# Optimization experiments

Measured on AMD Instinct MI355X. Metric: run time of the kernel, lower is better.

## Reference

```python
import jax, jax.numpy as jnp
import numpy as np

N_NODES = 50000
N_EDGES = 800000
NFEAT, NHID, NCLASS = 512, 128, 64


def setup_inputs() -> dict:
    key = jax.random.key(0)
    ks = jax.random.split(key, 8)
    x = jax.random.normal(ks[0], (N_NODES, NFEAT), dtype=jnp.float32)
    # GraphConvolution params (uniform-ish init like reset_parameters, stdv = 1/sqrt(fan_out))
    W1 = jax.random.normal(ks[1], (NFEAT, NHID), dtype=jnp.float32) * (1.0 / np.sqrt(NHID))
    b1 = jnp.zeros((NHID,), dtype=jnp.float32)
    W2 = jax.random.normal(ks[2], (NHID, NCLASS), dtype=jnp.float32) * (1.0 / np.sqrt(NCLASS))
    b2 = jnp.zeros((NCLASS,), dtype=jnp.float32)
    # sparse normalized adjacency in COO form
    edge_row = jax.random.randint(ks[3], (N_EDGES,), 0, N_NODES, dtype=jnp.int32)
    edge_col = jax.random.randint(ks[4], (N_EDGES,), 0, N_NODES, dtype=jnp.int32)
    edge_val = jax.random.uniform(ks[5], (N_EDGES,), dtype=jnp.float32) * 0.1
    return {"x": x, "W1": W1, "b1": b1, "W2": W2, "b2": b2,
            "edge_val": edge_val, "edge_row": edge_row, "edge_col": edge_col}


def _spmm(feat, edge_row, edge_col, edge_val, n_nodes):
    # (adj @ feat) with adj given as COO: out[r] = sum_e val[e] * feat[c[e]]
    msg = feat[edge_col] * edge_val[:, None]          # [E, d]
    return jax.ops.segment_sum(msg, edge_row, num_segments=n_nodes)


def reference(x, W1, b1, W2, b2, edge_val, edge_row, edge_col):
    # eval mode: dropout = identity, use_bn = False
    n = x.shape[0]
    h = jax.nn.relu(_spmm(x @ W1, edge_row, edge_col, edge_val, n) + b1)  # gc1 + relu
    out = _spmm(h @ W2, edge_row, edge_col, edge_val, n) + b2             # gc2
    return out
```

## Files before the change

### kernel.cpp

```cpp
#include <hip/hip_runtime.h>

#define N_NODES 50000
#define N_EDGES 800000
#define NFEAT 512
#define NHID 128
#define NCLASS 64

#define SCAN_BLOCKS 49
#define ZERO_BLOCKS 49

using bf16x8 = __attribute__((ext_vector_type(8))) __bf16;
using f32x4  = __attribute__((ext_vector_type(4))) float;
using u16x8  = __attribute__((ext_vector_type(8))) unsigned short;
using u16x4  = __attribute__((ext_vector_type(4))) unsigned short;
typedef unsigned long long u64;

__device__ __forceinline__ unsigned short f2bf(float f)
{
    unsigned u = __builtin_bit_cast(unsigned, f);
    unsigned r = (u + 0x7FFFu + ((u >> 16) & 1u)) >> 16;
    return (unsigned short)r;
}
__device__ __forceinline__ float bf2f(unsigned short b)
{
    return __builtin_bit_cast(float, (unsigned)b << 16);
}
__device__ __forceinline__ u16x4 cvt4(float4 f)
{
    u16x4 h;
    h[0] = __builtin_bit_cast(unsigned short, (__bf16)f.x);
    h[1] = __builtin_bit_cast(unsigned short, (__bf16)f.y);
    h[2] = __builtin_bit_cast(unsigned short, (__bf16)f.z);
    h[3] = __builtin_bit_cast(unsigned short, (__bf16)f.w);
    return h;
}

__global__ void prep_kernel(int4* __restrict__ zp, int n4,
                            const float* __restrict__ W1, const float* __restrict__ W2,
                            unsigned short* __restrict__ W1t, unsigned short* __restrict__ W2t)
{
    const int b = blockIdx.x;
    if (b < ZERO_BLOCKS) {
        const int i = b * 256 + threadIdx.x;
        if (i < n4) zp[i] = make_int4(0, 0, 0, 0);
    } else {
        const int idx = (b - ZERO_BLOCKS) * 256 + threadIdx.x;
        if (idx < NFEAT * NHID) {
            const int n = idx / NFEAT, k = idx % NFEAT;
            W1t[idx] = f2bf(W1[k * NHID + n]);
        } else {
            const int j = idx - NFEAT * NHID;
            if (j < NHID * NCLASS) {
                const int n = j / NHID, k = j % NHID;
                W2t[j] = f2bf(W2[k * NCLASS + n]);
            }
        }
    }
}

__global__ __launch_bounds__(512) void gemm1_pipe(const float* __restrict__ A,
                                                  const unsigned short* __restrict__ Bt,
                                                  unsigned short* __restrict__ C, int M)
{
    constexpr int K = NFEAT, N = NHID, BM = 128, BK = 32, NSTEP = K / BK;
    constexpr int LDW = BK + 8;
    __shared__ unsigned short As[2][BM][LDW];
    __shared__ unsigned short Bs[2][N][LDW];

    const int tid  = threadIdx.x;
    const int wid  = tid >> 6;
    const int lane = tid & 63;
    const int lm   = lane & 15;
    const int lk   = (lane >> 4) * 8;
    const int m0   = blockIdx.x * BM;

    const int ar0 = tid >> 3;
    const int ac0 = (tid & 7) * 4;
    const int ga0 = (m0 + ar0      < M) ? (m0 + ar0)      : (M - 1);
    const int ga1 = (m0 + ar0 + 64 < M) ? (m0 + ar0 + 64) : (M - 1);
    const float* Arow0 = &A[(size_t)ga0 * K];
    const float* Arow1 = &A[(size_t)ga1 * K];
    const int bn = tid >> 2;
    const int bk = (tid & 3) * 8;
    const unsigned short* Brow = &Bt[(size_t)bn * K];

    f32x4 acc[8] = {};

    {
        float4 fa0 = *(const float4*)&Arow0[ac0];
        float4 fa1 = *(const float4*)&Arow1[ac0];
        u16x8  bv  = *(const u16x8*)&Brow[bk];
        *(u16x4*)&As[0][ar0][ac0]      = cvt4(fa0);
        *(u16x4*)&As[0][ar0 + 64][ac0] = cvt4(fa1);
        *(u16x8*)&Bs[0][bn][bk]        = bv;
    }
    __syncthreads();

    #pragma unroll
    for (int t = 0; t < NSTEP; ++t) {
        const int cur = t & 1;
        float4 na0, na1; u16x8 nb;
        if (t + 1 < NSTEP) {
            na0 = *(const float4*)&Arow0[(t + 1) * BK + ac0];
            na1 = *(const float4*)&Arow1[(t + 1) * BK + ac0];
            nb  = *(const u16x8*)&Brow[(t + 1) * BK + bk];
        }
        bf16x8 a = __builtin_bit_cast(bf16x8, *(const u16x8*)&As[cur][wid * 16 + lm][lk]);
        #pragma unroll
        for (int nf = 0; nf < 8; ++nf) {
            bf16x8 b = __builtin_bit_cast(bf16x8, *(const u16x8*)&Bs[cur][nf * 16 + lm][lk]);
            acc[nf] = __builtin_amdgcn_mfma_f32_16x16x32_bf16(a, b, acc[nf], 0, 0, 0);
        }
        if (t + 1 < NSTEP) {
            *(u16x4*)&As[cur ^ 1][ar0][ac0]      = cvt4(na0);
            *(u16x4*)&As[cur ^ 1][ar0 + 64][ac0] = cvt4(na1);
            *(u16x8*)&Bs[cur ^ 1][bn][bk]        = nb;
            __syncthreads();
        }
    }

    #pragma unroll
    for (int nf = 0; nf < 8; ++nf)
        #pragma unroll
        for (int r = 0; r < 4; ++r) {
            const int m = m0 + wid * 16 + (lane >> 4) * 4 + r;
            if (m < M) C[(size_t)m * N + nf * 16 + lm] =
                __builtin_bit_cast(unsigned short, (__bf16)acc[nf][r]);
        }
}

template<int K, int N>
__global__ __launch_bounds__(256) void gemm_mfma_bf16a(const unsigned short* __restrict__ A,
                                                       const unsigned short* __restrict__ Bt,
                                                       unsigned short* __restrict__ C, int M)
{
    constexpr int BM = 128, BK = 32, NF = N / 16;
    constexpr int LDW = BK + 8;
    __shared__ unsigned short As[BM][LDW];
    __shared__ unsigned short Bs[N][LDW];

    const int tid  = threadIdx.x;
    const int wid  = tid >> 6;
    const int lane = tid & 63;
    const int lm   = lane & 15;
    const int lk   = (lane >> 4) * 8;
    const int m0   = blockIdx.x * BM;

    f32x4 acc[2][NF] = {};

    for (int k0 = 0; k0 < K; k0 += BK) {
        if (k0) __syncthreads();
        {
            #pragma unroll
            for (int c = 0; c < 2; ++c) {
                const int chunk = tid * 2 + c;
                const int r  = chunk >> 2;
                const int kc = (chunk & 3) * 8;
                const int m  = m0 + r;
                u16x8 v = {};
                if (m < M) v = *(const u16x8*)&A[(size_t)m * K + k0 + kc];
                *(u16x8*)&As[r][kc] = v;
            }
        }
        {
            constexpr int CH  = (N * BK / 8) / 256;
            constexpr int CPR = BK / 8;
            #pragma unroll
            for (int c = 0; c < CH; ++c) {
                const int chunk = tid * CH + c;
                const int n  = chunk / CPR;
                const int kc = (chunk % CPR) * 8;
                *(u16x8*)&Bs[n][kc] = *(const u16x8*)&Bt[(size_t)n * K + k0 + kc];
            }
        }
        __syncthreads();

        bf16x8 a[2];
        #pragma unroll
        for (int mf = 0; mf < 2; ++mf)
            a[mf] = __builtin_bit_cast(bf16x8, *(const u16x8*)&As[wid * 32 + mf * 16 + lm][lk]);
        #pragma unroll
        for (int nf = 0; nf < NF; ++nf) {
            bf16x8 b = __builtin_bit_cast(bf16x8, *(const u16x8*)&Bs[nf * 16 + lm][lk]);
            #pragma unroll
            for (int mf = 0; mf < 2; ++mf)
                acc[mf][nf] = __builtin_amdgcn_mfma_f32_16x16x32_bf16(a[mf], b, acc[mf][nf], 0, 0, 0);
        }
    }

    #pragma unroll
    for (int mf = 0; mf < 2; ++mf)
        #pragma unroll
        for (int nf = 0; nf < NF; ++nf)
            #pragma unroll
            for (int r = 0; r < 4; ++r) {
                const int m = m0 + wid * 32 + mf * 16 + (lane >> 4) * 4 + r;
                if (m < M) C[(size_t)m * N + nf * 16 + lm] =
                    __builtin_bit_cast(unsigned short, (__bf16)acc[mf][nf][r]);
            }
}

__global__ void hist_rank_kernel(const int* __restrict__ er, int* __restrict__ counts,
                                 unsigned char* __restrict__ rank)
{
    int e = blockIdx.x * blockDim.x + threadIdx.x;
    if (e < N_EDGES) rank[e] = (unsigned char)atomicAdd(&counts[er[e]], 1);
}

__global__ __launch_bounds__(1024) void scan_blocks(const int* __restrict__ counts,
                                                    int* __restrict__ row_ptr,
                                                    int* __restrict__ bsums)
{
    __shared__ int tmp[1024];
    const int tid = threadIdx.x;
    const int gid = blockIdx.x * 1024 + tid;
    const int v = (gid < N_NODES) ? counts[gid] : 0;
    tmp[tid] = v;
    __syncthreads();
    #pragma unroll
    for (int off = 1; off < 1024; off <<= 1) {
        int t = (tid >= off) ? tmp[tid - off] : 0;
        __syncthreads();
        tmp[tid] += t;
        __syncthreads();
    }
    if (gid < N_NODES) row_ptr[gid] = tmp[tid] - v;
    if (tid == 1023) bsums[blockIdx.x] = tmp[1023];
}

__global__ void scan_bsums(int* __restrict__ bsums)
{
    const int lane = threadIdx.x;
    const int orig = (lane < SCAN_BLOCKS) ? bsums[lane] : 0;
    int v = orig;
    #pragma unroll
    for (int off = 1; off < 64; off <<= 1) {
        int t = __shfl_up(v, off, 64);
        if (lane >= off) v += t;
    }
    if (lane < SCAN_BLOCKS) bsums[lane] = v - orig;
}

__global__ __launch_bounds__(1024) void add_offsets(int* __restrict__ row_ptr,
                                                    const int* __restrict__ bsums)
{
    const int gid = blockIdx.x * 1024 + threadIdx.x;
    if (gid < N_NODES) row_ptr[gid] += bsums[blockIdx.x];
    if (gid == 0) row_ptr[N_NODES] = N_EDGES;
}

__global__ void scatter_cv(const int* __restrict__ er, const int* __restrict__ ec,
                           const float* __restrict__ ev, const unsigned char* __restrict__ rank,
                           const int* __restrict__ row_ptr, unsigned* __restrict__ cv)
{
    int e = blockIdx.x * blockDim.x + threadIdx.x;
    if (e >= N_EDGES) return;
    const int r = er[e];
    const int pos = row_ptr[r] + (int)rank[e];
    cv[pos] = ((unsigned)f2bf(ev[e]) << 16) | (unsigned)ec[e];
}

__global__ __launch_bounds__(256) void spmm_bf16_h(const unsigned short* __restrict__ feat,
                                                   const int* __restrict__ row_ptr,
                                                   const unsigned* __restrict__ cv,
                                                   const float* __restrict__ bias,
                                                   unsigned short* __restrict__ out)
{
    const int wave = blockIdx.x * (blockDim.x >> 6) + (threadIdx.x >> 6);
    const int lane = threadIdx.x & 63;
    if (wave >= N_NODES) return;
    const int beg = row_ptr[wave];
    const int end = row_ptr[wave + 1];
    const int deg = end - beg;
    const int n1 = deg < 64 ? deg : 64;

    float ax[8] = {}, ay[8] = {};
    unsigned pcv = 0;
    if (lane < n1) pcv = cv[beg + lane];

    int u = 0;
    for (; u + 7 < n1; u += 8) {
        unsigned pp[8], ww[8];
        #pragma unroll
        for (int j = 0; j < 8; ++j) pp[j] = __shfl(pcv, u + j, 64);
        #pragma unroll
        for (int j = 0; j < 8; ++j)
            ww[j] = *(const unsigned*)&feat[(size_t)(pp[j] & 0xFFFFu) * NHID + lane * 2];
        #pragma unroll
        for (int j = 0; j < 8; ++j) {
            const float v = bf2f((unsigned short)(pp[j] >> 16));
            ax[j] += v * bf2f((unsigned short)(ww[j] & 0xFFFF));
            ay[j] += v * bf2f((unsigned short)(ww[j] >> 16));
        }
    }
    for (; u < n1; ++u) {
        const unsigned p = __shfl(pcv, u, 64);
        const float v = bf2f((unsigned short)(p >> 16));
        const unsigned w = *(const unsigned*)&feat[(size_t)(p & 0xFFFFu) * NHID + lane * 2];
        ax[u & 7] += v * bf2f((unsigned short)(w & 0xFFFF));
        ay[u & 7] += v * bf2f((unsigned short)(w >> 16));
    }
    for (int i = beg + 64; i < end; ++i) {
        const unsigned p = cv[i];
        const float v = bf2f((unsigned short)(p >> 16));
        const unsigned w = *(const unsigned*)&feat[(size_t)(p & 0xFFFFu) * NHID + lane * 2];
        ax[i & 7] += v * bf2f((unsigned short)(w & 0xFFFF));
        ay[i & 7] += v * bf2f((unsigned short)(w >> 16));
    }
    const float sx = ((ax[0] + ax[1]) + (ax[2] + ax[3])) + ((ax[4] + ax[5]) + (ax[6] + ax[7]));
    const float sy = ((ay[0] + ay[1]) + (ay[2] + ay[3])) + ((ay[4] + ay[5]) + (ay[6] + ay[7]));
    const float2 bb = *(const float2*)&bias[lane * 2];
    const float rx = fmaxf(sx + bb.x, 0.f);
    const float ry = fmaxf(sy + bb.y, 0.f);
    const unsigned pack = (unsigned)f2bf(rx) | ((unsigned)f2bf(ry) << 16);
    *(unsigned*)&out[(size_t)wave * NHID + lane * 2] = pack;
}

__global__ __launch_bounds__(256) void spmm_bf16_o(const unsigned short* __restrict__ feat,
                                                   const int* __restrict__ row_ptr,
                                                   const unsigned* __restrict__ cv,
                                                   const float* __restrict__ bias,
                                                   float* __restrict__ out)
{
    const int wave = blockIdx.x * (blockDim.x >> 6) + (threadIdx.x >> 6);
    const int lane = threadIdx.x & 63;
    if (wave >= N_NODES) return;
    const int beg = row_ptr[wave];
    const int end = row_ptr[wave + 1];
    const int deg = end - beg;
    const int n1 = deg < 64 ? deg : 64;

    float a[8] = {};
    unsigned pcv = 0;
    if (lane < n1) pcv = cv[beg + lane];

    int u = 0;
    for (; u + 7 < n1; u += 8) {
        unsigned pp[8]; unsigned short ww[8];
        #pragma unroll
        for (int j = 0; j < 8; ++j) pp[j] = __shfl(pcv, u + j, 64);
        #pragma unroll
        for (int j = 0; j < 8; ++j)
            ww[j] = feat[(size_t)(pp[j] & 0xFFFFu) * NCLASS + lane];
        #pragma unroll
        for (int j = 0; j < 8; ++j)
            a[j] += bf2f((unsigned short)(pp[j] >> 16)) * bf2f(ww[j]);
    }
    for (; u < n1; ++u) {
        const unsigned p = __shfl(pcv, u, 64);
        a[u & 7] += bf2f((unsigned short)(p >> 16)) * bf2f(feat[(size_t)(p & 0xFFFFu) * NCLASS + lane]);
    }
    for (int i = beg + 64; i < end; ++i) {
        const unsigned p = cv[i];
        a[i & 7] += bf2f((unsigned short)(p >> 16)) * bf2f(feat[(size_t)(p & 0xFFFFu) * NCLASS + lane]);
    }
    const float s = ((a[0] + a[1]) + (a[2] + a[3])) + ((a[4] + a[5]) + (a[6] + a[7]));
    out[(size_t)wave * NCLASS + lane] = s + bias[lane];
}

extern "C" void kernel_launch(void* const* d_in, const int* in_sizes, int n_in,
                              void* d_out, int out_size, void* d_ws, size_t ws_size,
                              hipStream_t stream)
{
    const float* x  = (const float*)d_in[0];
    const float* W1 = (const float*)d_in[1];
    const float* b1 = (const float*)d_in[2];
    const float* W2 = (const float*)d_in[3];
    const float* b2 = (const float*)d_in[4];
    const float* ev = (const float*)d_in[5];
    const int*   er = (const int*)d_in[6];
    const int*   ec = (const int*)d_in[7];
    float* out = (float*)d_out;

    unsigned* cv = (unsigned*)d_ws;
    unsigned char* rank = (unsigned char*)(cv + N_EDGES);
    unsigned short* XW1  = (unsigned short*)(rank + N_EDGES);
    unsigned short* Hpre = XW1 + (size_t)N_NODES * NHID;
    int* row_ptr = (int*)(Hpre + (size_t)N_NODES * NHID);
    int* counts  = row_ptr + 50016;
    int* bsums   = counts + 50016;
    unsigned short* W1t = (unsigned short*)(bsums + 64);
    unsigned short* W2t = W1t + NFEAT * NHID;

    unsigned short* HW2 = XW1;

    {
        const int n4 = (50016 + 64) / 4;
        const int conv_blocks = (NFEAT * NHID + NHID * NCLASS + 255) / 256;
        prep_kernel<<<ZERO_BLOCKS + conv_blocks, 256, 0, stream>>>(
            (int4*)counts, n4, W1, W2, W1t, W2t);
    }
    hist_rank_kernel<<<(N_EDGES + 255) / 256, 256, 0, stream>>>(er, counts, rank);
    scan_blocks<<<SCAN_BLOCKS, 1024, 0, stream>>>(counts, row_ptr, bsums);
    scan_bsums<<<1, 64, 0, stream>>>(bsums);
    add_offsets<<<SCAN_BLOCKS, 1024, 0, stream>>>(row_ptr, bsums);
    scatter_cv<<<(N_EDGES + 255) / 256, 256, 0, stream>>>(er, ec, ev, rank, row_ptr, cv);

    gemm1_pipe<<<(N_NODES + 127) / 128, 512, 0, stream>>>(x, W1t, XW1, N_NODES);
    spmm_bf16_h<<<(N_NODES + 3) / 4, 256, 0, stream>>>(XW1, row_ptr, cv, b1, Hpre);
    gemm_mfma_bf16a<NHID, NCLASS><<<(N_NODES + 127) / 128, 256, 0, stream>>>(Hpre, W2t, HW2, N_NODES);
    spmm_bf16_o<<<(N_NODES + 3) / 4, 256, 0, stream>>>(HW2, row_ptr, cv, b2, out);
}
```

Measured before the change: 164.2 us.

## Split SpMM lanes across edges with vectorized gathers; fuse block-sum scan into offset add

Both SpMM kernels now give each lane a 4-element (8-byte) slice of a feature row, so several edges are gathered per wave instruction (2 edges per wave for the hidden layer, 4 for the output layer). Partial sums are then combined with cross-lane shuffles. This cuts the number of gather instructions and shuffle broadcasts per edge and widens each memory access. The single-block bsums scan is folded into each add_offsets block, which drops one kernel launch at the cost of redundant per-block scans. The trade-off is extra reduction shuffles, masked lanes when degree is not a multiple of the group width, and half of the lanes sitting idle during the store.

```diff
diff --git a/kernel.cpp b/kernel.cpp
--- a/kernel.cpp
+++ b/kernel.cpp
@@ -228,24 +228,24 @@
     if (tid == 1023) bsums[blockIdx.x] = tmp[1023];
 }
 
-__global__ void scan_bsums(int* __restrict__ bsums)
-{
-    const int lane = threadIdx.x;
-    const int orig = (lane < SCAN_BLOCKS) ? bsums[lane] : 0;
-    int v = orig;
-    #pragma unroll
-    for (int off = 1; off < 64; off <<= 1) {
-        int t = __shfl_up(v, off, 64);
-        if (lane >= off) v += t;
-    }
-    if (lane < SCAN_BLOCKS) bsums[lane] = v - orig;
-}
-
-__global__ __launch_bounds__(1024) void add_offsets(int* __restrict__ row_ptr,
-                                                    const int* __restrict__ bsums)
-{
+__global__ __launch_bounds__(1024) void add_offsets2(int* __restrict__ row_ptr,
+                                                     const int* __restrict__ bsums)
+{
+    __shared__ int soff;
+    if (threadIdx.x < 64) {
+        const int lane = threadIdx.x;
+        const int orig = (lane < SCAN_BLOCKS) ? bsums[lane] : 0;
+        int v = orig;
+        #pragma unroll
+        for (int off = 1; off < 64; off <<= 1) {
+            int t = __shfl_up(v, off, 64);
+            if (lane >= off) v += t;
+        }
+        if (lane == (int)blockIdx.x) soff = v - orig;
+    }
+    __syncthreads();
     const int gid = blockIdx.x * 1024 + threadIdx.x;
-    if (gid < N_NODES) row_ptr[gid] += bsums[blockIdx.x];
+    if (gid < N_NODES) row_ptr[gid] += soff;
     if (gid == 0) row_ptr[N_NODES] = N_EDGES;
 }
 
@@ -274,46 +274,56 @@
     const int deg = end - beg;
     const int n1 = deg < 64 ? deg : 64;
 
-    float ax[8] = {}, ay[8] = {};
     unsigned pcv = 0;
     if (lane < n1) pcv = cv[beg + lane];
-
-    int u = 0;
-    for (; u + 7 < n1; u += 8) {
-        unsigned pp[8], ww[8];
-        #pragma unroll
-        for (int j = 0; j < 8; ++j) pp[j] = __shfl(pcv, u + j, 64);
-        #pragma unroll
-        for (int j = 0; j < 8; ++j)
-            ww[j] = *(const unsigned*)&feat[(size_t)(pp[j] & 0xFFFFu) * NHID + lane * 2];
-        #pragma unroll
-        for (int j = 0; j < 8; ++j) {
-            const float v = bf2f((unsigned short)(pp[j] >> 16));
-            ax[j] += v * bf2f((unsigned short)(ww[j] & 0xFFFF));
-            ay[j] += v * bf2f((unsigned short)(ww[j] >> 16));
-        }
-    }
-    for (; u < n1; ++u) {
-        const unsigned p = __shfl(pcv, u, 64);
-        const float v = bf2f((unsigned short)(p >> 16));
-        const unsigned w = *(const unsigned*)&feat[(size_t)(p & 0xFFFFu) * NHID + lane * 2];
-        ax[u & 7] += v * bf2f((unsigned short)(w & 0xFFFF));
-        ay[u & 7] += v * bf2f((unsigned short)(w >> 16));
-    }
-    for (int i = beg + 64; i < end; ++i) {
-        const unsigned p = cv[i];
-        const float v = bf2f((unsigned short)(p >> 16));
-        const unsigned w = *(const unsigned*)&feat[(size_t)(p & 0xFFFFu) * NHID + lane * 2];
-        ax[i & 7] += v * bf2f((unsigned short)(w & 0xFFFF));
-        ay[i & 7] += v * bf2f((unsigned short)(w >> 16));
-    }
-    const float sx = ((ax[0] + ax[1]) + (ax[2] + ax[3])) + ((ax[4] + ax[5]) + (ax[6] + ax[7]));
-    const float sy = ((ay[0] + ay[1]) + (ay[2] + ay[3])) + ((ay[4] + ay[5]) + (ay[6] + ay[7]));
-    const float2 bb = *(const float2*)&bias[lane * 2];
-    const float rx = fmaxf(sx + bb.x, 0.f);
-    const float ry = fmaxf(sy + bb.y, 0.f);
-    const unsigned pack = (unsigned)f2bf(rx) | ((unsigned)f2bf(ry) << 16);
-    *(unsigned*)&out[(size_t)wave * NHID + lane * 2] = pack;
+    const int half = lane >> 5;
+    const int qi   = (lane & 31) * 4;
+
+    float ax[4][4] = {};
+    for (int u = 0; u < n1; u += 8) {
+        unsigned p[4];
+        #pragma unroll
+        for (int g = 0; g < 4; ++g) {
+            const int idx = u + 2 * g + half;
+            const int s = idx < n1 ? idx : 0;
+            const unsigned t = __shfl(pcv, s, 64);
+            p[g] = (idx < n1) ? t : 0u;
+        }
+        u16x4 w[4];
+        #pragma unroll
+        for (int g = 0; g < 4; ++g)
+            w[g] = *(const u16x4*)&feat[(size_t)(p[g] & 0xFFFFu) * NHID + qi];
+        #pragma unroll
+        for (int g = 0; g < 4; ++g) {
+            const float v = bf2f((unsigned short)(p[g] >> 16));
+            #pragma unroll
+            for (int j = 0; j < 4; ++j)
+                ax[g][j] += v * bf2f(w[g][j]);
+        }
+    }
+    for (int i = beg + 64 + half; i < end; i += 2) {
+        const unsigned pp = cv[i];
+        const float v = bf2f((unsigned short)(pp >> 16));
+        const u16x4 w = *(const u16x4*)&feat[(size_t)(pp & 0xFFFFu) * NHID + qi];
+        #pragma unroll
+        for (int j = 0; j < 4; ++j) ax[0][j] += v * bf2f(w[j]);
+    }
+
+    float s[4];
+    #pragma unroll
+    for (int j = 0; j < 4; ++j) {
+        s[j] = (ax[0][j] + ax[1][j]) + (ax[2][j] + ax[3][j]);
+        s[j] += __shfl_xor(s[j], 32, 64);
+    }
+    if (half == 0) {
+        const float4 bb = *(const float4*)&bias[qi];
+        u16x4 o;
+        o[0] = __builtin_bit_cast(unsigned short, (__bf16)fmaxf(s[0] + bb.x, 0.f));
+        o[1] = __builtin_bit_cast(unsigned short, (__bf16)fmaxf(s[1] + bb.y, 0.f));
+        o[2] = __builtin_bit_cast(unsigned short, (__bf16)fmaxf(s[2] + bb.z, 0.f));
+        o[3] = __builtin_bit_cast(unsigned short, (__bf16)fmaxf(s[3] + bb.w, 0.f));
+        *(u16x4*)&out[(size_t)wave * NHID + qi] = o;
+    }
 }
 
 __global__ __launch_bounds__(256) void spmm_bf16_o(const unsigned short* __restrict__ feat,
@@ -330,32 +340,53 @@
     const int deg = end - beg;
     const int n1 = deg < 64 ? deg : 64;
 
-    float a[8] = {};
     unsigned pcv = 0;
     if (lane < n1) pcv = cv[beg + lane];
-
-    int u = 0;
-    for (; u + 7 < n1; u += 8) {
-        unsigned pp[8]; unsigned short ww[8];
-        #pragma unroll
-        for (int j = 0; j < 8; ++j) pp[j] = __shfl(pcv, u + j, 64);
-        #pragma unroll
-        for (int j = 0; j < 8; ++j)
-            ww[j] = feat[(size_t)(pp[j] & 0xFFFFu) * NCLASS + lane];
-        #pragma unroll
-        for (int j = 0; j < 8; ++j)
-            a[j] += bf2f((unsigned short)(pp[j] >> 16)) * bf2f(ww[j]);
-    }
-    for (; u < n1; ++u) {
-        const unsigned p = __shfl(pcv, u, 64);
-        a[u & 7] += bf2f((unsigned short)(p >> 16)) * bf2f(feat[(size_t)(p & 0xFFFFu) * NCLASS + lane]);
-    }
-    for (int i = beg + 64; i < end; ++i) {
-        const unsigned p = cv[i];
-        a[i & 7] += bf2f((unsigned short)(p >> 16)) * bf2f(feat[(size_t)(p & 0xFFFFu) * NCLASS + lane]);
-    }
-    const float s = ((a[0] + a[1]) + (a[2] + a[3])) + ((a[4] + a[5]) + (a[6] + a[7]));
-    out[(size_t)wave * NCLASS + lane] = s + bias[lane];
+    const int grp = lane >> 4;
+    const int qi  = (lane & 15) * 4;
+
+    float a[2][4] = {};
+    for (int u = 0; u < n1; u += 8) {
+        unsigned p[2];
+        #pragma unroll
+        for (int g = 0; g < 2; ++g) {
+            const int idx = u + 4 * g + grp;
+            const int s = idx < n1 ? idx : 0;
+            const unsigned t = __shfl(pcv, s, 64);
+            p[g] = (idx < n1) ? t : 0u;
+        }
+        u16x4 w[2];
+        #pragma unroll
+        for (int g = 0; g < 2; ++g)
+            w[g] = *(const u16x4*)&feat[(size_t)(p[g] & 0xFFFFu) * NCLASS + qi];
+        #pragma unroll
+        for (int g = 0; g < 2; ++g) {
+            const float v = bf2f((unsigned short)(p[g] >> 16));
+            #pragma unroll
+            for (int j = 0; j < 4; ++j)
+                a[g][j] += v * bf2f(w[g][j]);
+        }
+    }
+    for (int i = beg + 64 + grp; i < end; i += 4) {
+        const unsigned pp = cv[i];
+        const float v = bf2f((unsigned short)(pp >> 16));
+        const u16x4 w = *(const u16x4*)&feat[(size_t)(pp & 0xFFFFu) * NCLASS + qi];
+        #pragma unroll
+        for (int j = 0; j < 4; ++j) a[0][j] += v * bf2f(w[j]);
+    }
+
+    float s[4];
+    #pragma unroll
+    for (int j = 0; j < 4; ++j) {
+        s[j] = a[0][j] + a[1][j];
+        s[j] += __shfl_xor(s[j], 16, 64);
+        s[j] += __shfl_xor(s[j], 32, 64);
+    }
+    if (lane < 16) {
+        const float4 bb = *(const float4*)&bias[qi];
+        float4 o = make_float4(s[0] + bb.x, s[1] + bb.y, s[2] + bb.z, s[3] + bb.w);
+        *(float4*)&out[(size_t)wave * NCLASS + qi] = o;
+    }
 }
 
 extern "C" void kernel_launch(void* const* d_in, const int* in_sizes, int n_in,
@@ -392,8 +423,7 @@
     }
     hist_rank_kernel<<<(N_EDGES + 255) / 256, 256, 0, stream>>>(er, counts, rank);
     scan_blocks<<<SCAN_BLOCKS, 1024, 0, stream>>>(counts, row_ptr, bsums);
-    scan_bsums<<<1, 64, 0, stream>>>(bsums);
-    add_offsets<<<SCAN_BLOCKS, 1024, 0, stream>>>(row_ptr, bsums);
+    add_offsets2<<<SCAN_BLOCKS, 1024, 0, stream>>>(row_ptr, bsums);
     scatter_cv<<<(N_EDGES + 255) / 256, 256, 0, stream>>>(er, ec, ev, rank, row_ptr, cv);
 
     gemm1_pipe<<<(N_NODES + 127) / 128, 512, 0, stream>>>(x, W1t, XW1, N_NODES);
```

Result: faster. 148.7 us (-9.4%).
